# Kernel optimization log

Measured on AMD Instinct MI355X. Metric: run time of the kernel, lower is better.

The kernel has to match this reference:

```python
import jax, jax.numpy as jnp
import numpy as np

B, S, H = 8, 2048, 768

def setup_inputs() -> dict:
    key = jax.random.key(0)
    ks = jax.random.split(key, 11)
    queries = jax.random.normal(ks[0], (B, S, H), dtype=jnp.float32)
    keys_ = jax.random.normal(ks[1], (B, S, H), dtype=jnp.float32)
    values = jax.random.normal(ks[2], (B, S, H), dtype=jnp.float32)
    coordinates = jax.random.uniform(ks[3], (B, S, 2), dtype=jnp.float32)
    scale = 1.0 / np.sqrt(H)
    Wq = jax.random.normal(ks[4], (H, H), dtype=jnp.float32) * scale
    bq = jnp.zeros((H,), dtype=jnp.float32)
    Wk = jax.random.normal(ks[5], (H, H), dtype=jnp.float32) * scale
    bk = jnp.zeros((H,), dtype=jnp.float32)
    Wv = jax.random.normal(ks[6], (H, H), dtype=jnp.float32) * scale
    bv = jnp.zeros((H,), dtype=jnp.float32)
    spatial_weight = jax.random.normal(ks[7], (1,), dtype=jnp.float32)
    return {"queries": queries, "keys": keys_, "values": values,
            "coordinates": coordinates, "Wq": Wq, "bq": bq, "Wk": Wk,
            "bk": bk, "Wv": Wv, "bv": bv, "spatial_weight": spatial_weight}

def _cdist(c):
    # c: [B, S, 2] -> pairwise euclidean distances [B, S, S]
    sq = jnp.sum(c * c, axis=-1)  # [B, S]
    d2 = sq[:, :, None] + sq[:, None, :] - 2.0 * jnp.einsum('bsd,btd->bst', c, c)
    return jnp.sqrt(jnp.maximum(d2, 1e-12))

def reference(queries, keys, values, coordinates, Wq, bq, Wk, bk, Wv, bv, spatial_weight):
    q = queries @ Wq.T + bq  # [B, S, H]
    k = keys @ Wk.T + bk
    v = values @ Wv.T + bv
    scores = jnp.einsum('bsh,bth->bst', q, k)          # [B, S, S]
    scores = scores - spatial_weight[0] * _cdist(coordinates)
    attn = jax.nn.softmax(scores, axis=-1)
    out = jnp.einsum('bst,bth->bsh', attn, v)          # [B, S, H]
    return out, attn
```

## Files before the change

### kernel.cpp

```cpp
#include <hip/hip_runtime.h>
#include <stdint.h>


typedef _Float16 half8 __attribute__((ext_vector_type(8)));
typedef _Float16 half4v __attribute__((ext_vector_type(4)));
typedef float f32x4 __attribute__((ext_vector_type(4)));

#define DEVI static __device__ __forceinline__

constexpr int B_ = 8, S_ = 2048, H_ = 768;
constexpr long NX = (long)B_ * S_ * H_;
constexpr long NW = (long)H_ * H_;

DEVI void glds16(const void* g, void* l) {
  __builtin_amdgcn_global_load_lds(
      (const __attribute__((address_space(1))) uint32_t*)g,
      (__attribute__((address_space(3))) uint32_t*)l, 16, 0, 0);
}

DEVI void stage_tile(const _Float16* gbase, int rowStride, _Float16* lds, int tid) {
#pragma unroll
  for (int seg = 0; seg < 2; ++seg) {
    int u = seg * 256 + tid;
    int r = u >> 2, c = u & 3;
    int sc = c ^ ((r >> 1) & 3);
    glds16(gbase + (long)r * rowStride + sc * 8, lds + ((u & ~63) << 3));
  }
}

DEVI half8 frag(const _Float16* lds, int m0, int lane) {
  int row = m0 + (lane & 15);
  int c = (lane >> 4) ^ ((row >> 1) & 3);
  return *(const half8*)(lds + row * 32 + c * 8);
}

__global__ __launch_bounds__(256) void k_split(
    const float* __restrict__ xq, const float* __restrict__ xk,
    const float* __restrict__ xv, const float* __restrict__ wq,
    const float* __restrict__ wk, const float* __restrict__ wv,
    _Float16* __restrict__ dst) {
  const long NX4 = NX / 4, NW4 = NW / 4, TOT = 3 * NX4 + 3 * NW4;
  for (long u = (long)blockIdx.x * blockDim.x + threadIdx.x; u < TOT;
       u += (long)gridDim.x * blockDim.x) {
    const float4* src;
    _Float16 *dh, *dl;
    long idx;
    if (u < 3 * NX4) {
      int z = (u >= 2 * NX4) ? 2 : (u >= NX4) ? 1 : 0;
      idx = u - (long)z * NX4;
      src = (const float4*)(z == 0 ? xq : z == 1 ? xk : xv);
      dh = dst + (long)z * 2 * NX;
      dl = dh + NX;
    } else {
      long t = u - 3 * NX4;
      int z = (t >= 2 * NW4) ? 2 : (t >= NW4) ? 1 : 0;
      idx = t - (long)z * NW4;
      src = (const float4*)(z == 0 ? wq : z == 1 ? wk : wv);
      dh = dst + 6 * NX + (long)z * 2 * NW;
      dl = dh + NW;
    }
    float4 x = src[idx];
    half4v hi, lo;
    hi[0] = (_Float16)x.x; lo[0] = (_Float16)(x.x - (float)hi[0]);
    hi[1] = (_Float16)x.y; lo[1] = (_Float16)(x.y - (float)hi[1]);
    hi[2] = (_Float16)x.z; lo[2] = (_Float16)(x.z - (float)hi[2]);
    hi[3] = (_Float16)x.w; lo[3] = (_Float16)(x.w - (float)hi[3]);
    *(half4v*)(dh + idx * 4) = hi;
    *(half4v*)(dl + idx * 4) = lo;
  }
}

__global__ __launch_bounds__(256, 2) void k_proj(
    const _Float16* __restrict__ scratch, const float* __restrict__ bq,
    const float* __restrict__ bk, const float* __restrict__ bv,
    _Float16* __restrict__ qh, _Float16* __restrict__ ql,
    _Float16* __restrict__ kh, _Float16* __restrict__ kl,
    _Float16* __restrict__ vT) {
  const int nt = blockIdx.x, mt = blockIdx.y, z = blockIdx.z;
  const int tid = threadIdx.x;
  const bool full = (z < 2);
  const _Float16* Xh = scratch + (long)z * 2 * NX;
  const _Float16* Xl = Xh + NX;
  const _Float16* Wh = scratch + 6 * NX + (long)z * 2 * NW;
  const _Float16* Wl = Wh + NW;
  const float* bias = (z == 0) ? bq : (z == 1) ? bk : bv;

  __shared__ _Float16 sm[2][4][4096];

  f32x4 acc[4][4] = {};

  const _Float16* Ah = Xh + (long)(mt * 128) * H_;
  const _Float16* Al = Xl + (long)(mt * 128) * H_;
  const _Float16* Bh = Wh + (long)(nt * 128) * H_;
  const _Float16* Bl = Wl + (long)(nt * 128) * H_;

  stage_tile(Ah, H_, sm[0][0], tid);
  stage_tile(Bh, H_, sm[0][2], tid);
  if (full) {
    stage_tile(Al, H_, sm[0][1], tid);
    stage_tile(Bl, H_, sm[0][3], tid);
  }
  __syncthreads();

  const int lane = tid & 63, wid = tid >> 6;
  const int wm = (wid >> 1) * 64, wn = (wid & 1) * 64;

  int cur = 0;
  for (int kk = 0; kk < 24; ++kk) {
    if (kk + 1 < 24) {
      int o = (kk + 1) * 32;
      stage_tile(Ah + o, H_, sm[cur ^ 1][0], tid);
      stage_tile(Bh + o, H_, sm[cur ^ 1][2], tid);
      if (full) {
        stage_tile(Al + o, H_, sm[cur ^ 1][1], tid);
        stage_tile(Bl + o, H_, sm[cur ^ 1][3], tid);
      }
    }
    half8 ah[4], bh[4];
#pragma unroll
    for (int i = 0; i < 4; ++i) ah[i] = frag(sm[cur][0], wm + i * 16, lane);
#pragma unroll
    for (int j = 0; j < 4; ++j) bh[j] = frag(sm[cur][2], wn + j * 16, lane);
#pragma unroll
    for (int i = 0; i < 4; ++i)
#pragma unroll
      for (int j = 0; j < 4; ++j)
        acc[i][j] = __builtin_amdgcn_mfma_f32_16x16x32_f16(ah[i], bh[j],
                                                           acc[i][j], 0, 0, 0);
    if (full) {
      half8 al[4], bl[4];
#pragma unroll
      for (int i = 0; i < 4; ++i) al[i] = frag(sm[cur][1], wm + i * 16, lane);
#pragma unroll
      for (int j = 0; j < 4; ++j) bl[j] = frag(sm[cur][3], wn + j * 16, lane);
#pragma unroll
      for (int i = 0; i < 4; ++i)
#pragma unroll
        for (int j = 0; j < 4; ++j) {
          acc[i][j] = __builtin_amdgcn_mfma_f32_16x16x32_f16(ah[i], bl[j],
                                                             acc[i][j], 0, 0, 0);
          acc[i][j] = __builtin_amdgcn_mfma_f32_16x16x32_f16(al[i], bh[j],
                                                             acc[i][j], 0, 0, 0);
        }
    }
    __syncthreads();
    cur ^= 1;
  }

  _Float16* oh = (z == 0) ? qh : kh;
  _Float16* ol = (z == 0) ? ql : kl;
#pragma unroll
  for (int i = 0; i < 4; ++i) {
    int m_t = wm + i * 16 + ((lane >> 4) << 2);
#pragma unroll
    for (int j = 0; j < 4; ++j) {
      int n_t = wn + j * 16 + (lane & 15);
      int gn = nt * 128 + n_t;
      float bs = bias[gn];
      if (z < 2) {
#pragma unroll
        for (int r = 0; r < 4; ++r) {
          long gm = (long)mt * 128 + m_t + r;
          float y = acc[i][j][r] + bs;
          _Float16 hi = (_Float16)y;
          oh[gm * H_ + gn] = hi;
          ol[gm * H_ + gn] = (_Float16)(y - (float)hi);
        }
      } else {
        int gmI = mt * 128 + m_t;
        int bb = gmI >> 11, t0 = gmI & 2047;
        half4v pk;
#pragma unroll
        for (int r = 0; r < 4; ++r) pk[r] = (_Float16)(acc[i][j][r] + bs);
        *(half4v*)&vT[((long)bb * H_ + gn) * S_ + t0] = pk;
      }
    }
  }
}

__global__ __launch_bounds__(512, 2) void k_scores8(
    const _Float16* __restrict__ qh, const _Float16* __restrict__ ql,
    const _Float16* __restrict__ kh_, const _Float16* __restrict__ kl_,
    const float* __restrict__ coords, const float* __restrict__ sw,
    float* __restrict__ attn) {
  const int nt = blockIdx.x, mt = blockIdx.y, b = blockIdx.z;
  const int tid = threadIdx.x, lane = tid & 63, wid = tid >> 6;
  const int wr = wid >> 2, wc = wid & 3;

  __shared__ _Float16 lds[2][2][2][8192];
  __shared__ float cco[4][256];

  if (tid < 256) {
    long gi = (long)b * S_ + mt * 256 + tid;
    cco[0][tid] = coords[gi * 2 + 0];
    cco[1][tid] = coords[gi * 2 + 1];
  } else {
    int t = tid - 256;
    long gj = (long)b * S_ + nt * 256 + t;
    cco[2][t] = coords[gj * 2 + 0];
    cco[3][t] = coords[gj * 2 + 1];
  }
  const float w = sw[0];

  const long aoff = ((long)b * S_ + mt * 256) * H_;
  const long boff = ((long)b * S_ + nt * 256) * H_;

  long goff[2];
  int loff[2];
#pragma unroll
  for (int seg = 0; seg < 2; ++seg) {
    int u = seg * 512 + tid;
    int r = u >> 2, c = u & 3;
    int sc = c ^ ((r >> 1) & 3);
    goff[seg] = (long)r * H_ + sc * 8;
    loff[seg] = (u & ~63) << 3;
  }

  f32x4 acc[8][4] = {};

  auto asrc = [&](int kt) -> const _Float16* {
    int term = kt / 12, ko = (kt % 12) * 64;
    return (term == 2 ? ql : qh) + aoff + ko;
  };
  auto bsrc = [&](int kt) -> const _Float16* {
    int term = kt / 12, ko = (kt % 12) * 64;
    return (term == 1 ? kl_ : kh_) + boff + ko;
  };
  auto stg = [&](int kt, int chunk) {
    int khf = chunk >> 1, ab = chunk & 1;
    const _Float16* src = (ab ? bsrc(kt) : asrc(kt)) + khf * 32;
    _Float16* dst = &lds[kt & 1][khf][ab][0];
    glds16(src + goff[0], dst + loff[0]);
    glds16(src + goff[1], dst + loff[1]);
  };

  half8 bf[4];

  auto do_phase = [&](int slot, int kh, int mh, int sg_kt, int chunk, int vm) {
    const _Float16* A = &lds[slot][kh][0][0];
    const _Float16* Bt = &lds[slot][kh][1][0];
    half8 af[4];
    if (mh == 1) {
#pragma unroll
      for (int i = 0; i < 4; ++i)
        af[i] = frag(A, wr * 128 + mh * 64 + i * 16, lane);
    }
    if (sg_kt >= 0) stg(sg_kt, chunk);
    if (vm == 6) asm volatile("s_waitcnt vmcnt(6)" ::: "memory");
    else if (vm == 4) asm volatile("s_waitcnt vmcnt(4)" ::: "memory");
    else if (vm == 0) asm volatile("s_waitcnt vmcnt(0)" ::: "memory");
    __builtin_amdgcn_s_barrier();
    asm volatile("" ::: "memory");
    if (mh == 0) {
#pragma unroll
      for (int j = 0; j < 4; ++j) bf[j] = frag(Bt, wc * 64 + j * 16, lane);
#pragma unroll
      for (int i = 0; i < 4; ++i)
        af[i] = frag(A, wr * 128 + mh * 64 + i * 16, lane);
    }
    __builtin_amdgcn_s_setprio(1);
#pragma unroll
    for (int i = 0; i < 4; ++i)
#pragma unroll
      for (int j = 0; j < 4; ++j)
        acc[mh * 4 + i][j] = __builtin_amdgcn_mfma_f32_16x16x32_f16(
            af[i], bf[j], acc[mh * 4 + i][j], 0, 0, 0);
    __builtin_amdgcn_s_setprio(0);
    asm volatile("" ::: "memory");
    __builtin_amdgcn_s_barrier();
    asm volatile("" ::: "memory");
  };

  stg(0, 0); stg(0, 1); stg(0, 2); stg(0, 3);
  asm volatile("s_waitcnt vmcnt(0) lgkmcnt(0)" ::: "memory");
  __builtin_amdgcn_s_barrier();
  asm volatile("" ::: "memory");

#pragma unroll 1
  for (int g = 0; g < 35; ++g) {
    const int slot = g & 1;
    do_phase(slot, 0, 0, g + 1, 0, 6);
    do_phase(slot, 0, 1, g + 1, 1, -1);
    do_phase(slot, 1, 0, g + 1, 2, 6);
    do_phase(slot, 1, 1, g + 1, 3, -1);
  }
  do_phase(1, 0, 0, -1, 0, 4);
  do_phase(1, 0, 1, -1, 0, -1);
  do_phase(1, 1, 0, -1, 0, 0);
  do_phase(1, 1, 1, -1, 0, -1);

#pragma unroll
  for (int mi = 0; mi < 8; ++mi) {
    int m_t = wr * 128 + mi * 16 + ((lane >> 4) << 2);
#pragma unroll
    for (int j = 0; j < 4; ++j) {
      int n_t = wc * 64 + j * 16 + (lane & 15);
      float cjx = cco[2][n_t], cjy = cco[3][n_t];
      long rowbase = ((long)b * S_ + mt * 256 + m_t) * S_ + nt * 256 + n_t;
#pragma unroll
      for (int r = 0; r < 4; ++r) {
        float dx = cco[0][m_t + r] - cjx;
        float dy = cco[1][m_t + r] - cjy;
        float d = sqrtf(fmaxf(fmaf(dx, dx, dy * dy), 1e-12f));
        attn[rowbase + (long)r * S_] = acc[mi][j][r] - w * d;
      }
    }
  }
}

__global__ __launch_bounds__(256) void k_rowsoft(float* __restrict__ attn) {
  const int wid = threadIdx.x >> 6, lane = threadIdx.x & 63;
  float* p = attn + ((long)blockIdx.x * 4 + wid) * S_;
  float4 v[8];
#pragma unroll
  for (int i = 0; i < 8; ++i) v[i] = ((const float4*)p)[i * 64 + lane];
  float m = -3.4e38f;
#pragma unroll
  for (int i = 0; i < 8; ++i)
    m = fmaxf(m, fmaxf(fmaxf(v[i].x, v[i].y), fmaxf(v[i].z, v[i].w)));
#pragma unroll
  for (int o = 32; o > 0; o >>= 1) m = fmaxf(m, __shfl_xor(m, o));
  float l = 0.f;
#pragma unroll
  for (int i = 0; i < 8; ++i) {
    v[i].x = __expf(v[i].x - m);
    v[i].y = __expf(v[i].y - m);
    v[i].z = __expf(v[i].z - m);
    v[i].w = __expf(v[i].w - m);
    l += (v[i].x + v[i].y) + (v[i].z + v[i].w);
  }
#pragma unroll
  for (int o = 32; o > 0; o >>= 1) l += __shfl_xor(l, o);
  const float rl = 1.0f / l;
#pragma unroll
  for (int i = 0; i < 8; ++i) {
    v[i].x *= rl; v[i].y *= rl; v[i].z *= rl; v[i].w *= rl;
    ((float4*)p)[i * 64 + lane] = v[i];
  }
}

__global__ __launch_bounds__(256, 2) void k_pv(
    const float* __restrict__ attn, const _Float16* __restrict__ vT,
    float* __restrict__ outp) {
  const int nt = blockIdx.x, mt = blockIdx.y, b = blockIdx.z;
  const int tid = threadIdx.x;
  __shared__ _Float16 sm[2][2][4096];
  f32x4 acc[4][4] = {};
  const float* Ab = attn + ((long)b * S_ + mt * 128) * S_;
  const _Float16* Bb = vT + ((long)b * H_ + nt * 128) * S_;
  const int lane = tid & 63, wid = tid >> 6;
  const int wm = (wid >> 1) * 64, wn = (wid & 1) * 64;

  stage_tile(Bb, S_, sm[0][1], tid);
#pragma unroll
  for (int seg = 0; seg < 2; ++seg) {
    int u = seg * 256 + tid, r = u >> 2, c = u & 3;
    int sc = c ^ ((r >> 1) & 3);
    const float4* s4 = (const float4*)(Ab + (long)r * S_ + sc * 8);
    float4 x0 = s4[0], x1 = s4[1];
    half8 h = {(_Float16)x0.x, (_Float16)x0.y, (_Float16)x0.z, (_Float16)x0.w,
               (_Float16)x1.x, (_Float16)x1.y, (_Float16)x1.z, (_Float16)x1.w};
    *(half8*)(&sm[0][0][r * 32 + c * 8]) = h;
  }
  __syncthreads();

  int cur = 0;
  for (int kk = 0; kk < 64; ++kk) {
    float4 x0a, x1a, x0b, x1b;
    const bool pre = (kk + 1 < 64);
    if (pre) {
      stage_tile(Bb + (kk + 1) * 32, S_, sm[cur ^ 1][1], tid);
      {
        int u = tid, r = u >> 2, sc = (u & 3) ^ ((r >> 1) & 3);
        const float4* s4 =
            (const float4*)(Ab + (long)r * S_ + (kk + 1) * 32 + sc * 8);
        x0a = s4[0]; x1a = s4[1];
      }
      {
        int u = 256 + tid, r = u >> 2, sc = (u & 3) ^ ((r >> 1) & 3);
        const float4* s4 =
            (const float4*)(Ab + (long)r * S_ + (kk + 1) * 32 + sc * 8);
        x0b = s4[0]; x1b = s4[1];
      }
    }
    half8 ah[4], bh[4];
#pragma unroll
    for (int i = 0; i < 4; ++i) ah[i] = frag(sm[cur][0], wm + i * 16, lane);
#pragma unroll
    for (int j = 0; j < 4; ++j) bh[j] = frag(sm[cur][1], wn + j * 16, lane);
#pragma unroll
    for (int i = 0; i < 4; ++i)
#pragma unroll
      for (int j = 0; j < 4; ++j)
        acc[i][j] = __builtin_amdgcn_mfma_f32_16x16x32_f16(ah[i], bh[j],
                                                           acc[i][j], 0, 0, 0);
    if (pre) {
      {
        int u = tid, r = u >> 2, c = u & 3;
        half8 h = {(_Float16)x0a.x, (_Float16)x0a.y, (_Float16)x0a.z,
                   (_Float16)x0a.w, (_Float16)x1a.x, (_Float16)x1a.y,
                   (_Float16)x1a.z, (_Float16)x1a.w};
        *(half8*)(&sm[cur ^ 1][0][r * 32 + c * 8]) = h;
      }
      {
        int u = 256 + tid, r = u >> 2, c = u & 3;
        half8 h = {(_Float16)x0b.x, (_Float16)x0b.y, (_Float16)x0b.z,
                   (_Float16)x0b.w, (_Float16)x1b.x, (_Float16)x1b.y,
                   (_Float16)x1b.z, (_Float16)x1b.w};
        *(half8*)(&sm[cur ^ 1][0][r * 32 + c * 8]) = h;
      }
    }
    __syncthreads();
    cur ^= 1;
  }

#pragma unroll
  for (int i = 0; i < 4; ++i) {
    int m_t = wm + i * 16 + ((lane >> 4) << 2);
#pragma unroll
    for (int j = 0; j < 4; ++j) {
      int n_t = wn + j * 16 + (lane & 15);
      int h = nt * 128 + n_t;
      long rowbase = (long)b * S_ + mt * 128 + m_t;
#pragma unroll
      for (int r = 0; r < 4; ++r) outp[(rowbase + r) * H_ + h] = acc[i][j][r];
    }
  }
}

extern "C" void kernel_launch(void* const* d_in, const int* in_sizes, int n_in,
                              void* d_out, int out_size, void* d_ws,
                              size_t ws_size, hipStream_t stream) {
  const float* xq = (const float*)d_in[0];
  const float* xk = (const float*)d_in[1];
  const float* xv = (const float*)d_in[2];
  const float* co = (const float*)d_in[3];
  const float* wq = (const float*)d_in[4];
  const float* bq = (const float*)d_in[5];
  const float* wk = (const float*)d_in[6];
  const float* bk = (const float*)d_in[7];
  const float* wv = (const float*)d_in[8];
  const float* bv = (const float*)d_in[9];
  const float* sw = (const float*)d_in[10];

  float* out = (float*)d_out;
  float* attn = out + NX;
  _Float16* scratch = (_Float16*)d_out;

  _Float16* qh = (_Float16*)d_ws;
  _Float16* ql = qh + NX;
  _Float16* kh = ql + NX;
  _Float16* kl = kh + NX;
  _Float16* vT = kl + NX;

  k_split<<<dim3(2048), 256, 0, stream>>>(xq, xk, xv, wq, wk, wv, scratch);
  k_proj<<<dim3(6, 128, 3), 256, 0, stream>>>(scratch, bq, bk, bv, qh, ql, kh,
                                              kl, vT);
  k_scores8<<<dim3(8, 8, 8), 512, 0, stream>>>(qh, ql, kh, kl, co, sw, attn);
  k_rowsoft<<<dim3(4096), 256, 0, stream>>>(attn);
  k_pv<<<dim3(6, 16, 8), 256, 0, stream>>>(attn, vT, out);
}
```

Baseline: 553.9 us.

## Deepen scores pipeline, emit fp16 attention from softmax, skip unused V lo split

The scores kernel now stages K-chunks in half-tile units with a deeper prefetch (seven loads in flight) and an interleaved term ordering, with fragment loads moved ahead of the barrier. Softmax now also writes an fp16 copy of attention into the workspace that held Q, so the PV kernel can stream fp16 tiles straight to LDS via global_load_lds instead of loading fp32 and converting in registers. The split kernel stops writing the unused low half for V and its weights, which compacts the scratch layout. The cost is an extra fp16 attention write and more intricate wait-count bookkeeping.

```diff
diff --git a/kernel.cpp b/kernel.cpp
--- a/kernel.cpp
+++ b/kernel.cpp
@@ -11,6 +11,7 @@
 constexpr int B_ = 8, S_ = 2048, H_ = 768;
 constexpr long NX = (long)B_ * S_ * H_;
 constexpr long NW = (long)H_ * H_;
+constexpr long ATT = (long)B_ * S_ * S_;
 
 DEVI void glds16(const void* g, void* l) {
   __builtin_amdgcn_global_load_lds(
@@ -44,6 +45,7 @@
        u += (long)gridDim.x * blockDim.x) {
     const float4* src;
     _Float16 *dh, *dl;
+    bool wantLo = true;
     long idx;
     if (u < 3 * NX4) {
       int z = (u >= 2 * NX4) ? 2 : (u >= NX4) ? 1 : 0;
@@ -51,13 +53,15 @@
       src = (const float4*)(z == 0 ? xq : z == 1 ? xk : xv);
       dh = dst + (long)z * 2 * NX;
       dl = dh + NX;
+      wantLo = (z < 2);
     } else {
       long t = u - 3 * NX4;
       int z = (t >= 2 * NW4) ? 2 : (t >= NW4) ? 1 : 0;
       idx = t - (long)z * NW4;
       src = (const float4*)(z == 0 ? wq : z == 1 ? wk : wv);
-      dh = dst + 6 * NX + (long)z * 2 * NW;
+      dh = dst + 5 * NX + (long)z * 2 * NW;
       dl = dh + NW;
+      wantLo = (z < 2);
     }
     float4 x = src[idx];
     half4v hi, lo;
@@ -66,7 +70,7 @@
     hi[2] = (_Float16)x.z; lo[2] = (_Float16)(x.z - (float)hi[2]);
     hi[3] = (_Float16)x.w; lo[3] = (_Float16)(x.w - (float)hi[3]);
     *(half4v*)(dh + idx * 4) = hi;
-    *(half4v*)(dl + idx * 4) = lo;
+    if (wantLo) *(half4v*)(dl + idx * 4) = lo;
   }
 }
 
@@ -81,12 +85,11 @@
   const bool full = (z < 2);
   const _Float16* Xh = scratch + (long)z * 2 * NX;
   const _Float16* Xl = Xh + NX;
-  const _Float16* Wh = scratch + 6 * NX + (long)z * 2 * NW;
+  const _Float16* Wh = scratch + 5 * NX + (long)z * 2 * NW;
   const _Float16* Wl = Wh + NW;
   const float* bias = (z == 0) ? bq : (z == 1) ? bk : bv;
 
   __shared__ _Float16 sm[2][4][4096];
-
   f32x4 acc[4][4] = {};
 
   const _Float16* Ah = Xh + (long)(mt * 128) * H_;
@@ -157,7 +160,7 @@
       int n_t = wn + j * 16 + (lane & 15);
       int gn = nt * 128 + n_t;
       float bs = bias[gn];
-      if (z < 2) {
+      if (full) {
 #pragma unroll
         for (int r = 0; r < 4; ++r) {
           long gm = (long)mt * 128 + m_t + r;
@@ -178,7 +181,7 @@
   }
 }
 
-__global__ __launch_bounds__(512, 2) void k_scores8(
+__global__ __launch_bounds__(512, 2) void k_scores8p(
     const _Float16* __restrict__ qh, const _Float16* __restrict__ ql,
     const _Float16* __restrict__ kh_, const _Float16* __restrict__ kl_,
     const float* __restrict__ coords, const float* __restrict__ sw,
@@ -218,46 +221,37 @@
 
   f32x4 acc[8][4] = {};
 
-  auto asrc = [&](int kt) -> const _Float16* {
-    int term = kt / 12, ko = (kt % 12) * 64;
-    return (term == 2 ? ql : qh) + aoff + ko;
-  };
-  auto bsrc = [&](int kt) -> const _Float16* {
-    int term = kt / 12, ko = (kt % 12) * 64;
-    return (term == 1 ? kl_ : kh_) + boff + ko;
-  };
-  auto stg = [&](int kt, int chunk) {
-    int khf = chunk >> 1, ab = chunk & 1;
-    const _Float16* src = (ab ? bsrc(kt) : asrc(kt)) + khf * 32;
-    _Float16* dst = &lds[kt & 1][khf][ab][0];
+  auto stage_half = [&](int h) {
+    int th = h >> 2, kind = h & 3;
+    int khf = kind >> 1, mx = kind & 1;
+    int term = th % 3;
+    long ko = (long)(th / 3) * 64 + khf * 32;
+    const _Float16* src = mx ? ((term == 1 ? kl_ : kh_) + boff + ko)
+                             : ((term == 2 ? ql : qh) + aoff + ko);
+    _Float16* dst = &lds[th & 1][khf][mx][0];
     glds16(src + goff[0], dst + loff[0]);
     glds16(src + goff[1], dst + loff[1]);
   };
 
   half8 bf[4];
 
-  auto do_phase = [&](int slot, int kh, int mh, int sg_kt, int chunk, int vm) {
+  auto phase = [&](int slot, int kh, int mh, int hst, int vm) {
     const _Float16* A = &lds[slot][kh][0][0];
     const _Float16* Bt = &lds[slot][kh][1][0];
     half8 af[4];
-    if (mh == 1) {
-#pragma unroll
-      for (int i = 0; i < 4; ++i)
-        af[i] = frag(A, wr * 128 + mh * 64 + i * 16, lane);
-    }
-    if (sg_kt >= 0) stg(sg_kt, chunk);
+    if (mh == 0) {
+#pragma unroll
+      for (int j = 0; j < 4; ++j) bf[j] = frag(Bt, wc * 64 + j * 16, lane);
+    }
+#pragma unroll
+    for (int i = 0; i < 4; ++i)
+      af[i] = frag(A, wr * 128 + mh * 64 + i * 16, lane);
+    if (hst >= 0) stage_half(hst);
     if (vm == 6) asm volatile("s_waitcnt vmcnt(6)" ::: "memory");
-    else if (vm == 4) asm volatile("s_waitcnt vmcnt(4)" ::: "memory");
     else if (vm == 0) asm volatile("s_waitcnt vmcnt(0)" ::: "memory");
     __builtin_amdgcn_s_barrier();
-    asm volatile("" ::: "memory");
-    if (mh == 0) {
-#pragma unroll
-      for (int j = 0; j < 4; ++j) bf[j] = frag(Bt, wc * 64 + j * 16, lane);
-#pragma unroll
-      for (int i = 0; i < 4; ++i)
-        af[i] = frag(A, wr * 128 + mh * 64 + i * 16, lane);
-    }
+    asm volatile("s_waitcnt lgkmcnt(0)" ::: "memory");
+    __builtin_amdgcn_sched_barrier(0);
     __builtin_amdgcn_s_setprio(1);
 #pragma unroll
     for (int i = 0; i < 4; ++i)
@@ -268,26 +262,29 @@
     __builtin_amdgcn_s_setprio(0);
     asm volatile("" ::: "memory");
     __builtin_amdgcn_s_barrier();
-    asm volatile("" ::: "memory");
   };
 
-  stg(0, 0); stg(0, 1); stg(0, 2); stg(0, 3);
-  asm volatile("s_waitcnt vmcnt(0) lgkmcnt(0)" ::: "memory");
+#pragma unroll
+  for (int h = 0; h < 7; ++h) stage_half(h);
+  asm volatile("s_waitcnt vmcnt(6)" ::: "memory");
   __builtin_amdgcn_s_barrier();
-  asm volatile("" ::: "memory");
 
 #pragma unroll 1
-  for (int g = 0; g < 35; ++g) {
-    const int slot = g & 1;
-    do_phase(slot, 0, 0, g + 1, 0, 6);
-    do_phase(slot, 0, 1, g + 1, 1, -1);
-    do_phase(slot, 1, 0, g + 1, 2, 6);
-    do_phase(slot, 1, 1, g + 1, 3, -1);
-  }
-  do_phase(1, 0, 0, -1, 0, 4);
-  do_phase(1, 0, 1, -1, 0, -1);
-  do_phase(1, 1, 0, -1, 0, 0);
-  do_phase(1, 1, 1, -1, 0, -1);
+  for (int t = 0; t < 34; ++t) {
+    const int slot = t & 1, P = 4 * t;
+    phase(slot, 0, 0, P + 7, -1);
+    phase(slot, 0, 1, P + 8, -1);
+    phase(slot, 1, 0, P + 9, -1);
+    phase(slot, 1, 1, P + 10 <= 143 ? P + 10 : -1, 6);
+  }
+  phase(0, 0, 0, 143, -1);
+  phase(0, 0, 1, -1, -1);
+  phase(0, 1, 0, -1, -1);
+  phase(0, 1, 1, -1, 0);
+  phase(1, 0, 0, -1, -1);
+  phase(1, 0, 1, -1, -1);
+  phase(1, 1, 0, -1, -1);
+  phase(1, 1, 1, -1, -1);
 
 #pragma unroll
   for (int mi = 0; mi < 8; ++mi) {
@@ -308,9 +305,12 @@
   }
 }
 
-__global__ __launch_bounds__(256) void k_rowsoft(float* __restrict__ attn) {
+__global__ __launch_bounds__(256) void k_rowsoft(float* __restrict__ attn,
+                                                 _Float16* __restrict__ a16) {
   const int wid = threadIdx.x >> 6, lane = threadIdx.x & 63;
-  float* p = attn + ((long)blockIdx.x * 4 + wid) * S_;
+  long row = (long)blockIdx.x * 4 + wid;
+  float* p = attn + row * S_;
+  _Float16* p16 = a16 + row * S_;
   float4 v[8];
 #pragma unroll
   for (int i = 0; i < 8; ++i) v[i] = ((const float4*)p)[i * 64 + lane];
@@ -336,52 +336,32 @@
   for (int i = 0; i < 8; ++i) {
     v[i].x *= rl; v[i].y *= rl; v[i].z *= rl; v[i].w *= rl;
     ((float4*)p)[i * 64 + lane] = v[i];
-  }
-}
-
-__global__ __launch_bounds__(256, 2) void k_pv(
-    const float* __restrict__ attn, const _Float16* __restrict__ vT,
+    half4v h = {(_Float16)v[i].x, (_Float16)v[i].y, (_Float16)v[i].z,
+                (_Float16)v[i].w};
+    ((half4v*)p16)[i * 64 + lane] = h;
+  }
+}
+
+__global__ __launch_bounds__(256, 2) void k_pv16(
+    const _Float16* __restrict__ a16, const _Float16* __restrict__ vT,
     float* __restrict__ outp) {
   const int nt = blockIdx.x, mt = blockIdx.y, b = blockIdx.z;
-  const int tid = threadIdx.x;
+  const int tid = threadIdx.x, lane = tid & 63, wid = tid >> 6;
+  const int wm = (wid >> 1) * 64, wn = (wid & 1) * 64;
   __shared__ _Float16 sm[2][2][4096];
   f32x4 acc[4][4] = {};
-  const float* Ab = attn + ((long)b * S_ + mt * 128) * S_;
+  const _Float16* Ab = a16 + ((long)b * S_ + mt * 128) * S_;
   const _Float16* Bb = vT + ((long)b * H_ + nt * 128) * S_;
-  const int lane = tid & 63, wid = tid >> 6;
-  const int wm = (wid >> 1) * 64, wn = (wid & 1) * 64;
-
+
+  stage_tile(Ab, S_, sm[0][0], tid);
   stage_tile(Bb, S_, sm[0][1], tid);
-#pragma unroll
-  for (int seg = 0; seg < 2; ++seg) {
-    int u = seg * 256 + tid, r = u >> 2, c = u & 3;
-    int sc = c ^ ((r >> 1) & 3);
-    const float4* s4 = (const float4*)(Ab + (long)r * S_ + sc * 8);
-    float4 x0 = s4[0], x1 = s4[1];
-    half8 h = {(_Float16)x0.x, (_Float16)x0.y, (_Float16)x0.z, (_Float16)x0.w,
-               (_Float16)x1.x, (_Float16)x1.y, (_Float16)x1.z, (_Float16)x1.w};
-    *(half8*)(&sm[0][0][r * 32 + c * 8]) = h;
-  }
   __syncthreads();
 
   int cur = 0;
   for (int kk = 0; kk < 64; ++kk) {
-    float4 x0a, x1a, x0b, x1b;
-    const bool pre = (kk + 1 < 64);
-    if (pre) {
+    if (kk + 1 < 64) {
+      stage_tile(Ab + (kk + 1) * 32, S_, sm[cur ^ 1][0], tid);
       stage_tile(Bb + (kk + 1) * 32, S_, sm[cur ^ 1][1], tid);
-      {
-        int u = tid, r = u >> 2, sc = (u & 3) ^ ((r >> 1) & 3);
-        const float4* s4 =
-            (const float4*)(Ab + (long)r * S_ + (kk + 1) * 32 + sc * 8);
-        x0a = s4[0]; x1a = s4[1];
-      }
-      {
-        int u = 256 + tid, r = u >> 2, sc = (u & 3) ^ ((r >> 1) & 3);
-        const float4* s4 =
-            (const float4*)(Ab + (long)r * S_ + (kk + 1) * 32 + sc * 8);
-        x0b = s4[0]; x1b = s4[1];
-      }
     }
     half8 ah[4], bh[4];
 #pragma unroll
@@ -394,22 +374,6 @@
       for (int j = 0; j < 4; ++j)
         acc[i][j] = __builtin_amdgcn_mfma_f32_16x16x32_f16(ah[i], bh[j],
                                                            acc[i][j], 0, 0, 0);
-    if (pre) {
-      {
-        int u = tid, r = u >> 2, c = u & 3;
-        half8 h = {(_Float16)x0a.x, (_Float16)x0a.y, (_Float16)x0a.z,
-                   (_Float16)x0a.w, (_Float16)x1a.x, (_Float16)x1a.y,
-                   (_Float16)x1a.z, (_Float16)x1a.w};
-        *(half8*)(&sm[cur ^ 1][0][r * 32 + c * 8]) = h;
-      }
-      {
-        int u = 256 + tid, r = u >> 2, c = u & 3;
-        half8 h = {(_Float16)x0b.x, (_Float16)x0b.y, (_Float16)x0b.z,
-                   (_Float16)x0b.w, (_Float16)x1b.x, (_Float16)x1b.y,
-                   (_Float16)x1b.z, (_Float16)x1b.w};
-        *(half8*)(&sm[cur ^ 1][0][r * 32 + c * 8]) = h;
-      }
-    }
     __syncthreads();
     cur ^= 1;
   }
@@ -452,11 +416,12 @@
   _Float16* kh = ql + NX;
   _Float16* kl = kh + NX;
   _Float16* vT = kl + NX;
+  _Float16* a16 = qh;
 
   k_split<<<dim3(2048), 256, 0, stream>>>(xq, xk, xv, wq, wk, wv, scratch);
   k_proj<<<dim3(6, 128, 3), 256, 0, stream>>>(scratch, bq, bk, bv, qh, ql, kh,
                                               kl, vT);
-  k_scores8<<<dim3(8, 8, 8), 512, 0, stream>>>(qh, ql, kh, kl, co, sw, attn);
-  k_rowsoft<<<dim3(4096), 256, 0, stream>>>(attn);
-  k_pv<<<dim3(6, 16, 8), 256, 0, stream>>>(attn, vT, out);
-}
+  k_scores8p<<<dim3(8, 8, 8), 512, 0, stream>>>(qh, ql, kh, kl, co, sw, attn);
+  k_rowsoft<<<dim3(4096), 256, 0, stream>>>(attn, a16);
+  k_pv16<<<dim3(6, 16, 8), 256, 0, stream>>>(a16, vT, out);
+}
```

Measured after the change: 505.0 us. 8.8% less time.
